# Performance work log

Hardware: AMD Instinct MI355X
Metric: run time of the kernel (lower is better)

The kernel has to match this reference:

```python
import jax, jax.numpy as jnp
import numpy as np

N_NODES = 50000

def gcn_conv(x, src, dst, W, b, n):
    # PyG GCNConv: add self-loops, symmetric normalization, linear, aggregate, bias
    h = x @ W  # [n, out]
    loop = jnp.arange(n, dtype=src.dtype)
    si = jnp.concatenate([src, loop])
    di = jnp.concatenate([dst, loop])
    deg = jax.ops.segment_sum(jnp.ones_like(si, dtype=h.dtype), di, num_segments=n)
    dinv = jax.lax.rsqrt(jnp.maximum(deg, jnp.asarray(1.0, h.dtype)))  # deg>=1 with self-loops
    norm = dinv[si] * dinv[di]  # [E+n]
    out = jax.ops.segment_sum(h[si] * norm[:, None], di, num_segments=n)
    return out + b

def setup_inputs() -> dict:
    key = jax.random.key(0)
    ks = jax.random.split(key, 6)
    B, N, E = 1024, N_NODES, 800000
    gene_dim, hidden, feat = 256, 128, 64
    data = jax.random.normal(ks[0], (B, N), dtype=jnp.float32)
    x = jax.random.normal(ks[1], (N, gene_dim), dtype=jnp.float32)
    edge_index = jax.random.randint(ks[2], (2, E), 0, N, dtype=jnp.int64)
    W1 = jax.random.normal(ks[3], (gene_dim, hidden), dtype=jnp.float32) * 0.05
    b1 = jnp.zeros((hidden,), dtype=jnp.float32)
    W2 = jax.random.normal(ks[4], (hidden, feat), dtype=jnp.float32) * 0.05
    b2 = jnp.zeros((feat,), dtype=jnp.float32)
    return {"data": data, "x": x, "edge_index": edge_index,
            "W1": W1, "b1": b1, "W2": W2, "b2": b2}

def reference(data, x, edge_index, W1, b1, W2, b2):
    n = x.shape[0]
    src, dst = edge_index[0], edge_index[1]
    h = gcn_conv(x, src, dst, W1, b1, n)
    h = jax.nn.relu(h)
    h = gcn_conv(h, src, dst, W2, b2, n)
    return data @ h  # [B, feature_dim]
```

## Files before the change

kernel.cpp:

```cpp
#include <hip/hip_runtime.h>
#include <hip/hip_bf16.h>
#include <cstdint>

#define N_NODES 50000
#define N_EDGES 800000
#define GENE    256
#define HID     128
#define FEAT    64
#define NCHUNK  98
#define KC      256
#define KSPAN   512
#define NBKT    391
#define EB      128
#define EPB     6250

typedef __attribute__((ext_vector_type(8))) short bf16x8;
typedef __attribute__((ext_vector_type(4))) float f32x4;
typedef unsigned short u16;
typedef unsigned int u32;

__device__ __forceinline__ u16 f2b(float f) {
  __hip_bfloat16 h = __float2bfloat16(f);
  return *reinterpret_cast<u16*>(&h);
}
__device__ __forceinline__ float b2f(u16 u) {
  return __uint_as_float(((unsigned)u) << 16);
}
__device__ __forceinline__ float b2f_lo(u32 u) { return __uint_as_float(u << 16); }
__device__ __forceinline__ float b2f_hi(u32 u) { return __uint_as_float(u & 0xffff0000u); }

__device__ __forceinline__ bf16x8 cvt8(float4 f0, float4 f1) {
  bf16x8 a;
  a[0] = (short)f2b(f0.x); a[1] = (short)f2b(f0.y);
  a[2] = (short)f2b(f0.z); a[3] = (short)f2b(f0.w);
  a[4] = (short)f2b(f1.x); a[5] = (short)f2b(f1.y);
  a[6] = (short)f2b(f1.z); a[7] = (short)f2b(f1.w);
  return a;
}


__global__ void k_prep(const float* __restrict__ W1, u16* __restrict__ Wt1,
                       const float* __restrict__ W2, u16* __restrict__ Wt2) {
  int j = blockIdx.x * 256 + threadIdx.x;
  if (j < HID * GENE) {
    int n = j / GENE, k = j % GENE;
    Wt1[j] = f2b(W1[(size_t)k * HID + n]);
  }
  int j2 = j - HID * GENE;
  if (j2 >= 0 && j2 < FEAT * HID) {
    int n = j2 / HID, k = j2 % HID;
    Wt2[j2] = f2b(W2[(size_t)k * FEAT + n]);
  }
}


__global__ __launch_bounds__(256) void k_hist(const int* __restrict__ dst,
                                              u32* __restrict__ cntmat) {
  __shared__ u32 h[NBKT];
  int t = threadIdx.x;
  for (int i = t; i < NBKT; i += 256) h[i] = 0;
  __syncthreads();
  int e0 = blockIdx.x * EPB;
  for (int i = t; i < EPB; i += 256)
    atomicAdd(&h[dst[e0 + i] >> 7], 1u);
  __syncthreads();
  for (int i = t; i < NBKT; i += 256)
    cntmat[(size_t)blockIdx.x * NBKT + i] = h[i];
}

__global__ __launch_bounds__(512) void k_scanb(u32* __restrict__ cntmat,
                                               u32* __restrict__ bbase,
                                               int* __restrict__ row_ptr) {
  __shared__ u32 s[512];
  int t = threadIdx.x;
  u32 tot = 0;
  if (t < NBKT)
    for (int b = 0; b < EB; ++b) tot += cntmat[(size_t)b * NBKT + t];
  s[t] = tot;
  __syncthreads();
  for (int off = 1; off < 512; off <<= 1) {
    u32 add = (t >= off) ? s[t - off] : 0;
    __syncthreads();
    s[t] += add;
    __syncthreads();
  }
  u32 excl = s[t] - tot;
  if (t < NBKT) {
    bbase[t] = excl;
    u32 run = excl;
    for (int b = 0; b < EB; ++b) {
      u32 c = cntmat[(size_t)b * NBKT + t];
      cntmat[(size_t)b * NBKT + t] = run;
      run += c;
    }
  }
  if (t == 0) { bbase[NBKT] = (u32)N_EDGES; row_ptr[N_NODES] = N_EDGES; }
}

__global__ __launch_bounds__(256) void k_part(const int* __restrict__ src,
                                              const int* __restrict__ dst,
                                              const u32* __restrict__ offmat,
                                              u32* __restrict__ ebuf) {
  __shared__ u32 curs[NBKT];
  int t = threadIdx.x;
  for (int i = t; i < NBKT; i += 256)
    curs[i] = offmat[(size_t)blockIdx.x * NBKT + i];
  __syncthreads();
  int e0 = blockIdx.x * EPB;
  for (int i = t; i < EPB; i += 256) {
    int d = dst[e0 + i];
    int sc = src[e0 + i];
    u32 pos = atomicAdd(&curs[d >> 7], 1u);
    ebuf[pos] = ((u32)sc << 7) | (u32)(d & 127);
  }
}

__global__ __launch_bounds__(256) void k_bsort(const u32* __restrict__ ebuf,
                                               const u32* __restrict__ bbase,
                                               int* __restrict__ row_ptr,
                                               float* __restrict__ dinv,
                                               int* __restrict__ col) {
  __shared__ u32 cnt[128], cur[128], s[128];
  int t = threadIdx.x;
  int b = blockIdx.x;
  int base = (int)bbase[b], end = (int)bbase[b + 1];
  if (t < 128) cnt[t] = 0;
  __syncthreads();
  for (int e = base + t; e < end; e += 256)
    atomicAdd(&cnt[ebuf[e] & 127], 1u);
  __syncthreads();
  if (t < 128) s[t] = cnt[t];
  __syncthreads();
  for (int off = 1; off < 128; off <<= 1) {
    u32 add = 0;
    if (t < 128 && t >= off) add = s[t - off];
    __syncthreads();
    if (t < 128) s[t] += add;
    __syncthreads();
  }
  if (t < 128) {
    u32 excl = s[t] - cnt[t];
    int node = (b << 7) + t;
    if (node < N_NODES) {
      row_ptr[node] = base + (int)excl;
      dinv[node] = rsqrtf((float)(cnt[t] + 1));
    }
    cur[t] = excl;
  }
  __syncthreads();
  for (int e = base + t; e < end; e += 256) {
    u32 v = ebuf[e];
    u32 pos = atomicAdd(&cur[v & 127], 1u);
    col[base + (int)pos] = (int)(v >> 7);
  }
}


template<bool F32IN, int NN, int KK>
__global__ __launch_bounds__(256) void gemm_lds(const void* __restrict__ Xv,
                                                const u16* __restrict__ Wt,
                                                const float* __restrict__ dinv,
                                                u16* __restrict__ Y) {
  constexpr int NF = NN / 32;
  constexpr int KU = KK / 8;
  constexpr int UPT = NN * KK / 8 / 256;
  __shared__ u16 wlds[NN * KK];

  int t = threadIdx.x;
  int w = t >> 6, l = t & 63;
  int lm = l & 15, lg = l >> 4;
  int rowhalf = w >> 1, colhalf = w & 1;
  int m0 = blockIdx.x * 64;
  int cb = colhalf * (NN / 2);

#pragma unroll
  for (int i = 0; i < UPT; ++i) {
    int j = t + i * 256;
    int row = j / KU, u = j - row * KU;
    bf16x8 v = *(const bf16x8*)(Wt + j * 8);
    *(bf16x8*)((char*)wlds + row * (KK * 2) + ((u * 16) ^ ((row & 7) << 4))) = v;
  }
  __syncthreads();

  int ra0 = m0 + rowhalf * 32 + lm;
  int ra1 = ra0 + 16;
  int rs0 = (ra0 < N_NODES) ? ra0 : 0;
  int rs1 = (ra1 < N_NODES) ? ra1 : 0;

  f32x4 acc[2][NF] = {};
#pragma unroll
  for (int k0 = 0; k0 < KK; k0 += 32) {
    bf16x8 a0, a1;
    if constexpr (F32IN) {
      const float* x0 = (const float*)Xv + (size_t)rs0 * KK + k0 + lg * 8;
      const float* x1 = (const float*)Xv + (size_t)rs1 * KK + k0 + lg * 8;
      a0 = cvt8(*(const float4*)x0, *(const float4*)(x0 + 4));
      a1 = cvt8(*(const float4*)x1, *(const float4*)(x1 + 4));
    } else {
      a0 = *(const bf16x8*)((const u16*)Xv + (size_t)rs0 * KK + k0 + lg * 8);
      a1 = *(const bf16x8*)((const u16*)Xv + (size_t)rs1 * KK + k0 + lg * 8);
    }
#pragma unroll
    for (int f = 0; f < NF; ++f) {
      int row = cb + f * 16 + lm;
      bf16x8 b = *(const bf16x8*)((char*)wlds + row * (KK * 2) +
                                  (((k0 + lg * 8) * 2) ^ ((row & 7) << 4)));
      acc[0][f] = __builtin_amdgcn_mfma_f32_16x16x32_bf16(a0, b, acc[0][f], 0, 0, 0);
      acc[1][f] = __builtin_amdgcn_mfma_f32_16x16x32_bf16(a1, b, acc[1][f], 0, 0, 0);
    }
  }
#pragma unroll
  for (int rf = 0; rf < 2; ++rf) {
    int mo = m0 + rowhalf * 32 + rf * 16 + lg * 4;
#pragma unroll
    for (int r = 0; r < 4; ++r) {
      int mm = mo + r;
      if (mm < N_NODES) {
        float dv = dinv[mm];
#pragma unroll
        for (int f = 0; f < NF; ++f)
          Y[(size_t)mm * NN + cb + f * 16 + lm] = f2b(acc[rf][f][r] * dv);
      }
    }
  }
}


__global__ __launch_bounds__(256) void k_agg128(
    const u32* __restrict__ Ain, const float* __restrict__ dinv,
    const int* __restrict__ row_ptr, const int* __restrict__ col,
    const float* __restrict__ bias, u32* __restrict__ out) {
  int t = threadIdx.x;
  int node = blockIdx.x * 4 + (t >> 6);
  int l = t & 63;
  float2 bv = *(const float2*)(bias + 2 * l);

  float di = dinv[node];
  int beg = row_ptr[node], end = row_ptr[node + 1];
  u32 us = Ain[(size_t)node * 64 + l];
  float ax = b2f_lo(us), ay = b2f_hi(us);
  int r = beg;
  for (; r + 4 <= end; r += 4) {
    int s0 = col[r], s1 = col[r + 1], s2 = col[r + 2], s3 = col[r + 3];
    u32 u0 = Ain[(size_t)s0 * 64 + l];
    u32 u1 = Ain[(size_t)s1 * 64 + l];
    u32 u2 = Ain[(size_t)s2 * 64 + l];
    u32 u3 = Ain[(size_t)s3 * 64 + l];
    ax += (b2f_lo(u0) + b2f_lo(u1)) + (b2f_lo(u2) + b2f_lo(u3));
    ay += (b2f_hi(u0) + b2f_hi(u1)) + (b2f_hi(u2) + b2f_hi(u3));
  }
  for (; r < end; ++r) {
    u32 u0 = Ain[(size_t)col[r] * 64 + l];
    ax += b2f_lo(u0); ay += b2f_hi(u0);
  }
  float vx = fmaxf(bv.x + di * ax, 0.f);
  float vy = fmaxf(bv.y + di * ay, 0.f);
  out[(size_t)node * 64 + l] = ((u32)f2b(vy) << 16) | (u32)f2b(vx);
}


__global__ __launch_bounds__(256) void k_agg64(
    const u16* __restrict__ Ain, const float* __restrict__ dinv,
    const int* __restrict__ row_ptr, const int* __restrict__ col,
    const float* __restrict__ bias, u16* __restrict__ out) {
  int t = threadIdx.x;
  int node = blockIdx.x * 4 + (t >> 6);
  int f = t & 63;
  float bf = bias[f];

  float di = dinv[node];
  int beg = row_ptr[node], end = row_ptr[node + 1];
  float acc = b2f(Ain[(size_t)node * 64 + f]);
  int r = beg;
  for (; r + 4 <= end; r += 4) {
    int s0 = col[r], s1 = col[r + 1], s2 = col[r + 2], s3 = col[r + 3];
    float a0 = b2f(Ain[(size_t)s0 * 64 + f]);
    float a1 = b2f(Ain[(size_t)s1 * 64 + f]);
    float a2 = b2f(Ain[(size_t)s2 * 64 + f]);
    float a3 = b2f(Ain[(size_t)s3 * 64 + f]);
    acc += (a0 + a1) + (a2 + a3);
  }
  for (; r < end; ++r) acc += b2f(Ain[(size_t)col[r] * 64 + f]);
  out[(size_t)node * 64 + f] = f2b(bf + di * acc);
}


__global__ __launch_bounds__(256) void k_tr(const u16* __restrict__ h2,
                                            u16* __restrict__ h2t) {
  __shared__ u16 tile[64][65];
  int i0 = blockIdx.x * 64;
  int t = threadIdx.x;
  int r = t >> 2, c0 = (t & 3) * 16;
  int i = i0 + r;
#pragma unroll
  for (int j = 0; j < 16; ++j)
    tile[r][c0 + j] = (i < N_NODES) ? h2[(size_t)i * 64 + c0 + j] : (u16)0;
  __syncthreads();
  int io = t & 63, n0 = (t >> 6) * 16;
  int i2 = i0 + io;
  if (i2 < N_NODES) {
#pragma unroll
    for (int j = 0; j < 16; ++j)
      h2t[(size_t)(n0 + j) * N_NODES + i2] = tile[io][n0 + j];
  }
}


__global__ __launch_bounds__(256) void final_mfma(const float* __restrict__ data,
                                                  const u16* __restrict__ h2t,
                                                  float* __restrict__ partial) {
  constexpr int KU = KC / 8;
  __shared__ u16 blds[64 * KC];

  int t = threadIdx.x;
  int w = t >> 6, l = t & 63;
  int lm = l & 15, lg = l >> 4;
  int m = blockIdx.x * 64 + w * 16 + lm;
  f32x4 acc[4] = {};

  auto bload = [&](int koff, int f) -> bf16x8 {
    int row = f * 16 + lm;
    return *(const bf16x8*)((char*)blds + row * (KC * 2) +
                            ((koff * 2) ^ ((row & 7) << 4)));
  };

#pragma unroll
  for (int half = 0; half < 2; ++half) {
    int kc0 = blockIdx.y * KSPAN + half * KC;
    int klen = N_NODES - kc0; if (klen > KC) klen = KC;

    __syncthreads();
#pragma unroll
    for (int i = 0; i < 64 * KU / 256; ++i) {
      int j = t + i * 256;
      int row = j / KU, u = j - row * KU;
      int kpos = kc0 + u * 8;
      bf16x8 v = {};
      if (kpos + 8 <= N_NODES) v = *(const bf16x8*)(h2t + (size_t)row * N_NODES + kpos);
      *(bf16x8*)((char*)blds + row * (KC * 2) + ((u * 16) ^ ((row & 7) << 4))) = v;
    }
    __syncthreads();

    const float* drow = data + (size_t)m * N_NODES + kc0 + lg * 8;
    int kk = 0;
    for (; kk + 128 <= klen; kk += 128) {
      float4 fa[4][2];
#pragma unroll
      for (int s = 0; s < 4; ++s) {
        fa[s][0] = *(const float4*)(drow + kk + s * 32);
        fa[s][1] = *(const float4*)(drow + kk + s * 32 + 4);
      }
#pragma unroll
      for (int s = 0; s < 4; ++s) {
        bf16x8 a = cvt8(fa[s][0], fa[s][1]);
#pragma unroll
        for (int f = 0; f < 4; ++f)
          acc[f] = __builtin_amdgcn_mfma_f32_16x16x32_bf16(a, bload(kk + s * 32 + lg * 8, f), acc[f], 0, 0, 0);
      }
    }
    for (; kk + 32 <= klen; kk += 32) {
      bf16x8 a = cvt8(*(const float4*)(drow + kk), *(const float4*)(drow + kk + 4));
#pragma unroll
      for (int f = 0; f < 4; ++f)
        acc[f] = __builtin_amdgcn_mfma_f32_16x16x32_bf16(a, bload(kk + lg * 8, f), acc[f], 0, 0, 0);
    }
    if (kk < klen) {
      bool ok = (kk + lg * 8 + 8) <= klen;
      bf16x8 a = {};
      if (ok) a = cvt8(*(const float4*)(drow + kk), *(const float4*)(drow + kk + 4));
#pragma unroll
      for (int f = 0; f < 4; ++f)
        acc[f] = __builtin_amdgcn_mfma_f32_16x16x32_bf16(a, bload(kk + lg * 8, f), acc[f], 0, 0, 0);
    }
  }

  float* pout = partial + (size_t)blockIdx.y * (1024 * FEAT);
  int mo = blockIdx.x * 64 + w * 16 + lg * 4;
#pragma unroll
  for (int f = 0; f < 4; ++f)
#pragma unroll
    for (int r = 0; r < 4; ++r)
      pout[(size_t)(mo + r) * FEAT + f * 16 + lm] = acc[f][r];
}

__global__ __launch_bounds__(256) void k_red(const float* __restrict__ partial,
                                             float* __restrict__ out) {
  int i = blockIdx.x * 256 + threadIdx.x;
  f32x4 s = {};
#pragma unroll
  for (int c = 0; c < NCHUNK; ++c)
    s += *(const f32x4*)(partial + (size_t)c * (1024 * FEAT) + i * 4);
  *(f32x4*)((float*)out + i * 4) = s;
}


extern "C" void kernel_launch(void* const* d_in, const int* in_sizes, int n_in,
                              void* d_out, int out_size, void* d_ws, size_t ws_size,
                              hipStream_t stream) {
  const float* data = (const float*)d_in[0];
  const float* x    = (const float*)d_in[1];
  const int*   ei   = (const int*)d_in[2];
  const float* W1   = (const float*)d_in[3];
  const float* b1   = (const float*)d_in[4];
  const float* W2   = (const float*)d_in[5];
  const float* b2   = (const float*)d_in[6];
  float* out = (float*)d_out;

  char* ws = (char*)d_ws;
  u16*   A      = (u16*)(ws + 0);
  u16*   Hb     = (u16*)(ws + 12800000);
  u16*   h2t    = (u16*)(ws + 25690112);
  u16*   Wt1    = (u16*)(ws + 32090112);
  u16*   Wt2    = (u16*)(ws + 32155648);
  int*   rowp   = (int*)(ws + 32172032);
  float* dinv   = (float*)(ws + 32372048);
  int*   col    = (int*)(ws + 32572048);
  u32*   ebuf   = (u32*)(ws + 35772048);
  u32*   cntmat = (u32*)(ws + 38972048);
  u32*   bbase  = (u32*)(ws + 39172240);
  float* part   = (float*)(ws + 39173808);

  const int* srcp = ei;
  const int* dstp = ei + N_EDGES;

  k_prep<<<(HID * GENE + FEAT * HID + 255) / 256, 256, 0, stream>>>(W1, Wt1, W2, Wt2);

  k_hist<<<EB, 256, 0, stream>>>(dstp, cntmat);
  k_scanb<<<1, 512, 0, stream>>>(cntmat, bbase, rowp);
  k_part<<<EB, 256, 0, stream>>>(srcp, dstp, cntmat, ebuf);
  k_bsort<<<NBKT, 256, 0, stream>>>(ebuf, bbase, rowp, dinv, col);

  gemm_lds<true, HID, GENE><<<(N_NODES + 63) / 64, 256, 0, stream>>>(x, Wt1, dinv, A);
  k_agg128<<<N_NODES / 4, 256, 0, stream>>>((const u32*)A, dinv, rowp, col, b1, (u32*)Hb);

  gemm_lds<false, FEAT, HID><<<(N_NODES + 63) / 64, 256, 0, stream>>>(Hb, Wt2, dinv, A);
  k_agg64<<<N_NODES / 4, 256, 0, stream>>>(A, dinv, rowp, col, b2, Hb);

  k_tr<<<(N_NODES + 63) / 64, 256, 0, stream>>>(Hb, h2t);

  final_mfma<<<dim3(16, NCHUNK), 256, 0, stream>>>(data, h2t, part);
  k_red<<<(1024 * FEAT) / 4 / 256, 256, 0, stream>>>(part, out);
}
```

Baseline: 224.1 us.

## Fuse layer-2 aggregation with transpose, merge prep into histogram, deepen gather unroll

```diff
diff --git a/kernel.cpp b/kernel.cpp
--- a/kernel.cpp
+++ b/kernel.cpp
@@ -39,33 +39,33 @@
 }
 
 
-__global__ void k_prep(const float* __restrict__ W1, u16* __restrict__ Wt1,
-                       const float* __restrict__ W2, u16* __restrict__ Wt2) {
-  int j = blockIdx.x * 256 + threadIdx.x;
-  if (j < HID * GENE) {
-    int n = j / GENE, k = j % GENE;
-    Wt1[j] = f2b(W1[(size_t)k * HID + n]);
-  }
-  int j2 = j - HID * GENE;
-  if (j2 >= 0 && j2 < FEAT * HID) {
-    int n = j2 / HID, k = j2 % HID;
-    Wt2[j2] = f2b(W2[(size_t)k * FEAT + n]);
-  }
-}
-
-
-__global__ __launch_bounds__(256) void k_hist(const int* __restrict__ dst,
-                                              u32* __restrict__ cntmat) {
+__global__ __launch_bounds__(256) void k_prep_hist(
+    const int* __restrict__ dst, u32* __restrict__ cntmat,
+    const float* __restrict__ W1, u16* __restrict__ Wt1,
+    const float* __restrict__ W2, u16* __restrict__ Wt2) {
   __shared__ u32 h[NBKT];
   int t = threadIdx.x;
-  for (int i = t; i < NBKT; i += 256) h[i] = 0;
-  __syncthreads();
-  int e0 = blockIdx.x * EPB;
-  for (int i = t; i < EPB; i += 256)
-    atomicAdd(&h[dst[e0 + i] >> 7], 1u);
-  __syncthreads();
-  for (int i = t; i < NBKT; i += 256)
-    cntmat[(size_t)blockIdx.x * NBKT + i] = h[i];
+  if (blockIdx.x < EB) {
+    for (int i = t; i < NBKT; i += 256) h[i] = 0;
+    __syncthreads();
+    int e0 = blockIdx.x * EPB;
+    for (int i = t; i < EPB; i += 256)
+      atomicAdd(&h[dst[e0 + i] >> 7], 1u);
+    __syncthreads();
+    for (int i = t; i < NBKT; i += 256)
+      cntmat[(size_t)blockIdx.x * NBKT + i] = h[i];
+  } else {
+    int j = (blockIdx.x - EB) * 256 + t;
+    if (j < HID * GENE) {
+      int n = j / GENE, k = j % GENE;
+      Wt1[j] = f2b(W1[(size_t)k * HID + n]);
+    }
+    int j2 = j - HID * GENE;
+    if (j2 >= 0 && j2 < FEAT * HID) {
+      int n = j2 / HID, k = j2 % HID;
+      Wt2[j2] = f2b(W2[(size_t)k * FEAT + n]);
+    }
+  }
 }
 
 __global__ __launch_bounds__(512) void k_scanb(u32* __restrict__ cntmat,
@@ -240,12 +240,25 @@
   u32 us = Ain[(size_t)node * 64 + l];
   float ax = b2f_lo(us), ay = b2f_hi(us);
   int r = beg;
+  for (; r + 8 <= end; r += 8) {
+    u32 u0 = Ain[(size_t)col[r]     * 64 + l];
+    u32 u1 = Ain[(size_t)col[r + 1] * 64 + l];
+    u32 u2 = Ain[(size_t)col[r + 2] * 64 + l];
+    u32 u3 = Ain[(size_t)col[r + 3] * 64 + l];
+    u32 u4 = Ain[(size_t)col[r + 4] * 64 + l];
+    u32 u5 = Ain[(size_t)col[r + 5] * 64 + l];
+    u32 u6 = Ain[(size_t)col[r + 6] * 64 + l];
+    u32 u7 = Ain[(size_t)col[r + 7] * 64 + l];
+    ax += ((b2f_lo(u0) + b2f_lo(u1)) + (b2f_lo(u2) + b2f_lo(u3))) +
+          ((b2f_lo(u4) + b2f_lo(u5)) + (b2f_lo(u6) + b2f_lo(u7)));
+    ay += ((b2f_hi(u0) + b2f_hi(u1)) + (b2f_hi(u2) + b2f_hi(u3))) +
+          ((b2f_hi(u4) + b2f_hi(u5)) + (b2f_hi(u6) + b2f_hi(u7)));
+  }
   for (; r + 4 <= end; r += 4) {
-    int s0 = col[r], s1 = col[r + 1], s2 = col[r + 2], s3 = col[r + 3];
-    u32 u0 = Ain[(size_t)s0 * 64 + l];
-    u32 u1 = Ain[(size_t)s1 * 64 + l];
-    u32 u2 = Ain[(size_t)s2 * 64 + l];
-    u32 u3 = Ain[(size_t)s3 * 64 + l];
+    u32 u0 = Ain[(size_t)col[r]     * 64 + l];
+    u32 u1 = Ain[(size_t)col[r + 1] * 64 + l];
+    u32 u2 = Ain[(size_t)col[r + 2] * 64 + l];
+    u32 u3 = Ain[(size_t)col[r + 3] * 64 + l];
     ax += (b2f_lo(u0) + b2f_lo(u1)) + (b2f_lo(u2) + b2f_lo(u3));
     ay += (b2f_hi(u0) + b2f_hi(u1)) + (b2f_hi(u2) + b2f_hi(u3));
   }
@@ -259,49 +272,57 @@
 }
 
 
-__global__ __launch_bounds__(256) void k_agg64(
+__global__ __launch_bounds__(256) void k_agg64t(
     const u16* __restrict__ Ain, const float* __restrict__ dinv,
     const int* __restrict__ row_ptr, const int* __restrict__ col,
-    const float* __restrict__ bias, u16* __restrict__ out) {
-  int t = threadIdx.x;
-  int node = blockIdx.x * 4 + (t >> 6);
-  int f = t & 63;
+    const float* __restrict__ bias, u16* __restrict__ h2t) {
+  __shared__ u16 tile[64][34];
+  int t = threadIdx.x;
+  int w = t >> 6, f = t & 63;
+  int base = blockIdx.x * 32;
   float bf = bias[f];
 
-  float di = dinv[node];
-  int beg = row_ptr[node], end = row_ptr[node + 1];
-  float acc = b2f(Ain[(size_t)node * 64 + f]);
-  int r = beg;
-  for (; r + 4 <= end; r += 4) {
-    int s0 = col[r], s1 = col[r + 1], s2 = col[r + 2], s3 = col[r + 3];
-    float a0 = b2f(Ain[(size_t)s0 * 64 + f]);
-    float a1 = b2f(Ain[(size_t)s1 * 64 + f]);
-    float a2 = b2f(Ain[(size_t)s2 * 64 + f]);
-    float a3 = b2f(Ain[(size_t)s3 * 64 + f]);
-    acc += (a0 + a1) + (a2 + a3);
-  }
-  for (; r < end; ++r) acc += b2f(Ain[(size_t)col[r] * 64 + f]);
-  out[(size_t)node * 64 + f] = f2b(bf + di * acc);
-}
-
-
-__global__ __launch_bounds__(256) void k_tr(const u16* __restrict__ h2,
-                                            u16* __restrict__ h2t) {
-  __shared__ u16 tile[64][65];
-  int i0 = blockIdx.x * 64;
-  int t = threadIdx.x;
-  int r = t >> 2, c0 = (t & 3) * 16;
-  int i = i0 + r;
-#pragma unroll
-  for (int j = 0; j < 16; ++j)
-    tile[r][c0 + j] = (i < N_NODES) ? h2[(size_t)i * 64 + c0 + j] : (u16)0;
-  __syncthreads();
-  int io = t & 63, n0 = (t >> 6) * 16;
-  int i2 = i0 + io;
-  if (i2 < N_NODES) {
-#pragma unroll
-    for (int j = 0; j < 16; ++j)
-      h2t[(size_t)(n0 + j) * N_NODES + i2] = tile[io][n0 + j];
+  for (int n = 0; n < 8; ++n) {
+    int node = base + w * 8 + n;
+    if (node < N_NODES) {
+      float di = dinv[node];
+      int beg = row_ptr[node], end = row_ptr[node + 1];
+      float acc = b2f(Ain[(size_t)node * 64 + f]);
+      int r = beg;
+      for (; r + 8 <= end; r += 8) {
+        float a0 = b2f(Ain[(size_t)col[r]     * 64 + f]);
+        float a1 = b2f(Ain[(size_t)col[r + 1] * 64 + f]);
+        float a2 = b2f(Ain[(size_t)col[r + 2] * 64 + f]);
+        float a3 = b2f(Ain[(size_t)col[r + 3] * 64 + f]);
+        float a4 = b2f(Ain[(size_t)col[r + 4] * 64 + f]);
+        float a5 = b2f(Ain[(size_t)col[r + 5] * 64 + f]);
+        float a6 = b2f(Ain[(size_t)col[r + 6] * 64 + f]);
+        float a7 = b2f(Ain[(size_t)col[r + 7] * 64 + f]);
+        acc += ((a0 + a1) + (a2 + a3)) + ((a4 + a5) + (a6 + a7));
+      }
+      for (; r + 4 <= end; r += 4) {
+        float a0 = b2f(Ain[(size_t)col[r]     * 64 + f]);
+        float a1 = b2f(Ain[(size_t)col[r + 1] * 64 + f]);
+        float a2 = b2f(Ain[(size_t)col[r + 2] * 64 + f]);
+        float a3 = b2f(Ain[(size_t)col[r + 3] * 64 + f]);
+        acc += (a0 + a1) + (a2 + a3);
+      }
+      for (; r < end; ++r) acc += b2f(Ain[(size_t)col[r] * 64 + f]);
+      tile[f][w * 8 + n] = f2b(bf + di * acc);
+    }
+  }
+  __syncthreads();
+
+  int row = t >> 2, cg = t & 3;
+  int c0 = base + cg * 8;
+  if (c0 + 8 <= N_NODES) {
+    u16 tmp[8];
+#pragma unroll
+    for (int j = 0; j < 8; ++j) tmp[j] = tile[row][cg * 8 + j];
+    *(int4*)(h2t + (size_t)row * N_NODES + c0) = *(const int4*)tmp;
+  } else {
+    for (int j = 0; j < 8 && c0 + j < N_NODES; ++j)
+      h2t[(size_t)row * N_NODES + c0 + j] = tile[row][cg * 8 + j];
   }
 }
 
@@ -423,9 +444,9 @@
   const int* srcp = ei;
   const int* dstp = ei + N_EDGES;
 
-  k_prep<<<(HID * GENE + FEAT * HID + 255) / 256, 256, 0, stream>>>(W1, Wt1, W2, Wt2);
-
-  k_hist<<<EB, 256, 0, stream>>>(dstp, cntmat);
+  const int PREPB = (HID * GENE + FEAT * HID + 255) / 256;
+
+  k_prep_hist<<<EB + PREPB, 256, 0, stream>>>(dstp, cntmat, W1, Wt1, W2, Wt2);
   k_scanb<<<1, 512, 0, stream>>>(cntmat, bbase, rowp);
   k_part<<<EB, 256, 0, stream>>>(srcp, dstp, cntmat, ebuf);
   k_bsort<<<NBKT, 256, 0, stream>>>(ebuf, bbase, rowp, dinv, col);
@@ -434,9 +455,7 @@
   k_agg128<<<N_NODES / 4, 256, 0, stream>>>((const u32*)A, dinv, rowp, col, b1, (u32*)Hb);
 
   gemm_lds<false, FEAT, HID><<<(N_NODES + 63) / 64, 256, 0, stream>>>(Hb, Wt2, dinv, A);
-  k_agg64<<<N_NODES / 4, 256, 0, stream>>>(A, dinv, rowp, col, b2, Hb);
-
-  k_tr<<<(N_NODES + 63) / 64, 256, 0, stream>>>(Hb, h2t);
+  k_agg64t<<<(N_NODES + 31) / 32, 256, 0, stream>>>(A, dinv, rowp, col, b2, h2t);
 
   final_mfma<<<dim3(16, NCHUNK), 256, 0, stream>>>(data, h2t, part);
   k_red<<<(1024 * FEAT) / 4 / 256, 256, 0, stream>>>(part, out);
```

Result: faster. 205.2 us (-8.4%).
